# Performance work log

Measured on AMD Instinct MI355X. Metric: run time of the kernel, lower is better.

## Reference

```python
import math
import jax, jax.numpy as jnp
import numpy as np

EPS = 1e-8
N_ITER = 5


def _partial_ot(C, reg):
    # C: (M, N) cost matrix. Faithful to partial_optimal_transport with
    # diag-matmuls replaced by equivalent broadcast row/col scaling.
    M, N = C.shape
    a = jnp.full((M,), 1.0 / M, dtype=C.dtype)
    b = jnp.full((N,), 1.0 / N, dtype=C.dtype)
    m = jnp.minimum(a.sum(), b.sum())  # = 1.0 here
    K = jnp.exp(-C / jnp.clip(reg, EPS))
    K = K * (m / jnp.clip(K.sum(), EPS))

    def body(K, _):
        r = jnp.minimum(a / jnp.clip(K.sum(axis=1), EPS), 1.0)   # min(a/rowsum, dx)
        K1 = r[:, None] * K
        c = jnp.minimum(b / jnp.clip(K1.sum(axis=0), EPS), 1.0)  # min(b/colsum, dy)
        K2 = K1 * c[None, :]
        K = K2 * (m / jnp.clip(K2.sum(), EPS))
        return K, None

    K, _ = jax.lax.scan(body, K, None, length=N_ITER)
    return K


def _rigid_transform(a, b, w):
    # a: (M,3) source points, b: (M,3) weighted targets, w: (M,) weights
    wn = w[:, None] / (w.sum() + 1e-6)            # normalized weights (M,1)
    centroid_a = (a * wn).sum(axis=0)             # (3,)
    centroid_b = (b * wn).sum(axis=0)
    ac = a - centroid_a
    bc = b - centroid_b
    cov = ac.T @ (bc * wn)                        # (3,3)
    u, s, vh = jnp.linalg.svd(cov, full_matrices=False)
    v = vh.T                                      # torch.svd's V
    rot_pos = v @ u.T
    v_neg = v.at[:, 2].multiply(-1.0)
    rot_neg = v_neg @ u.T
    det = jnp.linalg.det(rot_pos)
    rot = jnp.where(det > 0, rot_pos, rot_neg)
    trans = -rot @ centroid_a + centroid_b        # (3,)
    return jnp.concatenate([rot, trans[:, None]], axis=1)  # (3,4)


def _one_sample(se, te, s, t, rho):
    # se: (D,M) src feats, te: (D,N) tgt feats, s: (3,M), t: (3,N)
    D = se.shape[0]
    scores = (se.T @ te) / math.sqrt(D)           # (M,N)
    C = -jax.nn.log_softmax(scores, axis=1)
    matches = _partial_ot(C, rho)                 # (M,N)
    rowsum = matches.sum(axis=1, keepdims=True)   # (M,1)
    weighted_ref = (matches @ t.T) / (rowsum + 1e-6)  # (M,3)
    T = _rigid_transform(s.T, weighted_ref, rowsum[:, 0])
    return T, matches


def _forward(src_embedding, tgt_embedding, src, tgt, rho):
    Ts, match_mats = jax.vmap(_one_sample, in_axes=(0, 0, 0, 0, None))(
        src_embedding, tgt_embedding, src, tgt, rho)
    return Ts[:, :3, :3], Ts[:, :3, 3], match_mats


def setup_inputs() -> dict:
    key = jax.random.key(0)
    k1, k2, k3, k4 = jax.random.split(key, 4)
    B, D, M, N = 16, 256, 2048, 2048
    return {
        "src_embedding": jax.random.normal(k1, (B, D, M), dtype=jnp.float32),
        "tgt_embedding": jax.random.normal(k2, (B, D, N), dtype=jnp.float32),
        "src": jax.random.normal(k3, (B, 3, M), dtype=jnp.float32),
        "tgt": jax.random.normal(k4, (B, 3, N), dtype=jnp.float32),
        "rho": jnp.asarray(1.0, dtype=jnp.float32),
    }


def reference(src_embedding, tgt_embedding, src, tgt, rho):
    return _forward(src_embedding, tgt_embedding, src, tgt, rho)
```

## Files before the change

kernel.cpp:

```cpp
#include <hip/hip_runtime.h>
#include <math.h>

#define B_ 16
#define D_ 256
#define M_ 2048
#define N_ 2048
#define EPSF 1e-8f
#define AVAL (1.0f/2048.0f)

typedef __bf16  bf16x8 __attribute__((ext_vector_type(8)));
typedef float   f32x4  __attribute__((ext_vector_type(4)));

__device__ __forceinline__ float wredsum(float x){
  #pragma unroll
  for (int off=32; off; off>>=1) x += __shfl_xor(x, off);
  return x;
}
__device__ __forceinline__ float wredmax(float x){
  #pragma unroll
  for (int off=32; off; off>>=1) x = fmaxf(x, __shfl_xor(x, off));
  return x;
}
__device__ __forceinline__ unsigned short f2bf(float x){
  unsigned int v = __float_as_uint(x);
  unsigned int r = (v + 0x7fffu + ((v>>16)&1u)) >> 16;
  return (unsigned short)r;
}
__device__ __forceinline__ float bf2f(unsigned short u){ return __uint_as_float(((unsigned int)u)<<16); }
__device__ __forceinline__ float h2f(unsigned short h){
  _Float16 x; __builtin_memcpy(&x,&h,2); return (float)x;
}
__device__ __forceinline__ unsigned short f2h(float x){
  _Float16 h = (_Float16)x; unsigned short u; __builtin_memcpy(&u,&h,2); return u;
}

__device__ __forceinline__ void gll16(const void* gsrc, void* ldst){
  __builtin_amdgcn_global_load_lds(
      (const __attribute__((address_space(1))) unsigned int*)gsrc,
      (__attribute__((address_space(3))) unsigned int*)(unsigned int)(unsigned long long)ldst,
      16, 0, 0);
}

__global__ __launch_bounds__(256) void convert_kernel(const float* __restrict__ se,
                                                      const float* __restrict__ te,
                                                      uint4* __restrict__ Ah, uint4* __restrict__ Al,
                                                      uint4* __restrict__ Bh, uint4* __restrict__ Bl)
{
  const int t  = threadIdx.x;
  const int mb = blockIdx.x;
  const int g  = blockIdx.y;
  const int z  = blockIdx.z;
  const int b  = z & 15, op = z >> 4;
  const int m  = mb*256 + t;
  const float* src = (op ? te : se) + (size_t)b*D_*M_ + (size_t)g*8*M_ + m;
  float x[8];
  #pragma unroll
  for (int j=0;j<8;j++) x[j] = src[(size_t)j*M_];
  unsigned int hw[4], lw[4];
  #pragma unroll
  for (int p=0;p<4;p++){
    float a0 = x[2*p], a1 = x[2*p+1];
    unsigned short h0 = f2bf(a0), h1 = f2bf(a1);
    unsigned short q0 = f2bf(a0 - bf2f(h0)), q1 = f2bf(a1 - bf2f(h1));
    hw[p] = (unsigned)h0 | ((unsigned)h1<<16);
    lw[p] = (unsigned)q0 | ((unsigned)q1<<16);
  }
  const size_t gi = (size_t)(b*32 + g)*2048 + m;
  uint4* Ph = op ? Bh : Ah;
  uint4* Pl = op ? Bl : Al;
  Ph[gi] = *(const uint4*)hw;
  Pl[gi] = *(const uint4*)lw;
}

__global__ __launch_bounds__(256) void gemm_fast(const uint4* __restrict__ Ah,
                                                 const uint4* __restrict__ Al,
                                                 const uint4* __restrict__ Bh,
                                                 const uint4* __restrict__ Bl,
                                                 float* __restrict__ S)
{
  __shared__ unsigned int sAh[2048], sAl[2048], sBh[2048], sBl[2048];
  const int b  = blockIdx.z;
  const int mb = blockIdx.y;
  const int nb = blockIdx.x;
  const int t    = threadIdx.x;
  const int wave = t >> 6, lane = t & 63;
  const int wy = wave >> 1, wx = wave & 1;
  const int quad = lane >> 4, l15 = lane & 15;

  f32x4 acc[4][4] = {};

  for (int kc=0; kc<8; kc++){
    __syncthreads();
    #pragma unroll
    for (int r=0;r<2;r++){
      const int i  = r*256 + t;
      const int gq = i >> 7, m = i & 127;
      const size_t rowg = (size_t)(b*32 + kc*4 + gq)*2048;
      gll16(Ah + rowg + mb*128 + m, (char*)sAh + (size_t)i*16);
      gll16(Al + rowg + mb*128 + m, (char*)sAl + (size_t)i*16);
      gll16(Bh + rowg + nb*128 + m, (char*)sBh + (size_t)i*16);
      gll16(Bl + rowg + nb*128 + m, (char*)sBl + (size_t)i*16);
    }
    __syncthreads();
    bf16x8 ah[4], al[4], bh[4], bl[4];
    #pragma unroll
    for (int rt=0;rt<4;rt++){
      int ra = (quad*128 + wy*64 + rt*16 + l15)*4;
      int rb = (quad*128 + wx*64 + rt*16 + l15)*4;
      ah[rt] = *(const bf16x8*)&sAh[ra];
      al[rt] = *(const bf16x8*)&sAl[ra];
      bh[rt] = *(const bf16x8*)&sBh[rb];
      bl[rt] = *(const bf16x8*)&sBl[rb];
    }
    #pragma unroll
    for (int rt=0;rt<4;rt++)
      #pragma unroll
      for (int ct=0;ct<4;ct++){
        acc[rt][ct] = __builtin_amdgcn_mfma_f32_16x16x32_bf16(ah[rt], bh[ct], acc[rt][ct], 0,0,0);
        acc[rt][ct] = __builtin_amdgcn_mfma_f32_16x16x32_bf16(ah[rt], bl[ct], acc[rt][ct], 0,0,0);
        acc[rt][ct] = __builtin_amdgcn_mfma_f32_16x16x32_bf16(al[rt], bh[ct], acc[rt][ct], 0,0,0);
      }
  }
  const float sc = 0.0625f;
  #pragma unroll
  for (int rt=0;rt<4;rt++){
    #pragma unroll
    for (int r=0;r<4;r++){
      int m = mb*128 + wy*64 + rt*16 + quad*4 + r;
      float* rowp = S + (size_t)(b*M_ + m)*N_;
      #pragma unroll
      for (int ct=0;ct<4;ct++){
        int n = nb*128 + wx*64 + ct*16 + l15;
        rowp[n] = acc[rt][ct][r] * sc;
      }
    }
  }
}

__global__ __launch_bounds__(256) void gemm_kernel(const float* __restrict__ se,
                                                   const float* __restrict__ te,
                                                   float* __restrict__ S)
{
  __shared__ unsigned int Ah[2048], Al[2048], Bh[2048], Bl[2048];
  const int b  = blockIdx.z;
  const int mb = blockIdx.y;
  const int nb = blockIdx.x;
  const int t    = threadIdx.x;
  const int wave = t >> 6, lane = t & 63;
  const int wy = wave >> 1, wx = wave & 1;
  const int quad = lane >> 4, l15 = lane & 15;
  const int ml  = t & 127;
  const int dh  = t >> 7;

  f32x4 acc[4][4] = {};

  const float* Abase = se + (size_t)b*D_*M_ + mb*128 + ml;
  const float* Bbase = te + (size_t)b*D_*M_ + nb*128 + ml;

  for (int kc=0; kc<8; kc++){
    __syncthreads();
    {
      float x[16];
      #pragma unroll
      for (int j=0;j<16;j++) x[j] = Abase[(size_t)(kc*32 + dh*16 + j)*M_];
      #pragma unroll
      for (int gi=0; gi<2; gi++){
        unsigned int hw[4], lw[4];
        #pragma unroll
        for (int p=0;p<4;p++){
          float a0 = x[gi*8+2*p], a1 = x[gi*8+2*p+1];
          unsigned short h0 = f2bf(a0), h1 = f2bf(a1);
          unsigned short q0 = f2bf(a0 - bf2f(h0)), q1 = f2bf(a1 - bf2f(h1));
          hw[p] = (unsigned)h0 | ((unsigned)h1<<16);
          lw[p] = (unsigned)q0 | ((unsigned)q1<<16);
        }
        int idx = ((dh*2+gi)*128 + ml)*4;
        *(uint4*)&Ah[idx] = *(uint4*)hw;
        *(uint4*)&Al[idx] = *(uint4*)lw;
      }
    }
    {
      float x[16];
      #pragma unroll
      for (int j=0;j<16;j++) x[j] = Bbase[(size_t)(kc*32 + dh*16 + j)*M_];
      #pragma unroll
      for (int gi=0; gi<2; gi++){
        unsigned int hw[4], lw[4];
        #pragma unroll
        for (int p=0;p<4;p++){
          float a0 = x[gi*8+2*p], a1 = x[gi*8+2*p+1];
          unsigned short h0 = f2bf(a0), h1 = f2bf(a1);
          unsigned short q0 = f2bf(a0 - bf2f(h0)), q1 = f2bf(a1 - bf2f(h1));
          hw[p] = (unsigned)h0 | ((unsigned)h1<<16);
          lw[p] = (unsigned)q0 | ((unsigned)q1<<16);
        }
        int idx = ((dh*2+gi)*128 + ml)*4;
        *(uint4*)&Bh[idx] = *(uint4*)hw;
        *(uint4*)&Bl[idx] = *(uint4*)lw;
      }
    }
    __syncthreads();
    bf16x8 ah[4], al[4], bh[4], bl[4];
    #pragma unroll
    for (int rt=0;rt<4;rt++){
      int ra = (quad*128 + wy*64 + rt*16 + l15)*4;
      int rb = (quad*128 + wx*64 + rt*16 + l15)*4;
      ah[rt] = *(const bf16x8*)&Ah[ra];
      al[rt] = *(const bf16x8*)&Al[ra];
      bh[rt] = *(const bf16x8*)&Bh[rb];
      bl[rt] = *(const bf16x8*)&Bl[rb];
    }
    #pragma unroll
    for (int rt=0;rt<4;rt++)
      #pragma unroll
      for (int ct=0;ct<4;ct++){
        acc[rt][ct] = __builtin_amdgcn_mfma_f32_16x16x32_bf16(ah[rt], bh[ct], acc[rt][ct], 0,0,0);
        acc[rt][ct] = __builtin_amdgcn_mfma_f32_16x16x32_bf16(ah[rt], bl[ct], acc[rt][ct], 0,0,0);
        acc[rt][ct] = __builtin_amdgcn_mfma_f32_16x16x32_bf16(al[rt], bh[ct], acc[rt][ct], 0,0,0);
      }
  }
  const float sc = 0.0625f;
  #pragma unroll
  for (int rt=0;rt<4;rt++){
    #pragma unroll
    for (int r=0;r<4;r++){
      int m = mb*128 + wy*64 + rt*16 + quad*4 + r;
      float* rowp = S + (size_t)(b*M_ + m)*N_;
      #pragma unroll
      for (int ct=0;ct<4;ct++){
        int n = nb*128 + wx*64 + ct*16 + l15;
        rowp[n] = acc[rt][ct][r] * sc;
      }
    }
  }
}

__global__ __launch_bounds__(256) void stats_kernel(float* __restrict__ S,
                                                    const float* __restrict__ rho,
                                                    float* __restrict__ lse,
                                                    float* __restrict__ y0)
{
  const int b = blockIdx.y;
  const int m = blockIdx.x*4 + (threadIdx.x>>6);
  const int lane = threadIdx.x & 63;
  const float invrho = 1.0f / fmaxf(rho[0], EPSF);
  float* row = S + (size_t)(b*M_ + m)*N_;
  const float4* row4 = (const float4*)row;
  float4 vals[8];
  float mx = -3.4e38f;
  #pragma unroll
  for (int k=0;k<8;k++){
    float4 v = row4[lane + 64*k];
    vals[k] = v;
    mx = fmaxf(mx, fmaxf(fmaxf(v.x,v.y), fmaxf(v.z,v.w)));
  }
  mx = wredmax(mx);
  float e1=0.0f;
  #pragma unroll
  for (int k=0;k<8;k++){
    float4 v = vals[k];
    e1 += __expf(v.x-mx)+__expf(v.y-mx)+__expf(v.z-mx)+__expf(v.w-mx);
  }
  e1 = wredsum(e1);
  const float l = mx + __logf(e1);
  uint2* rowh2 = (uint2*)row;
  float y2 = 0.0f;
  #pragma unroll
  for (int k=0;k<8;k++){
    float4 v = vals[k];
    unsigned short h0 = f2h(__expf((v.x-l)*invrho));
    unsigned short h1 = f2h(__expf((v.y-l)*invrho));
    unsigned short h2 = f2h(__expf((v.z-l)*invrho));
    unsigned short h3 = f2h(__expf((v.w-l)*invrho));
    y2 += h2f(h0)+h2f(h1)+h2f(h2)+h2f(h3);
    uint2 pk;
    pk.x = (unsigned)h0 | ((unsigned)h1<<16);
    pk.y = (unsigned)h2 | ((unsigned)h3<<16);
    rowh2[lane + 64*k] = pk;
  }
  y2 = wredsum(y2);
  if (lane==0){
    lse[b*M_+m] = l;
    y0 [b*M_+m] = y2;
  }
}

__global__ __launch_bounds__(256) void init_kernel(const float* __restrict__ y0,
                                                   float* __restrict__ u, float* __restrict__ v,
                                                   float* __restrict__ w, float* __restrict__ g)
{
  const int b = blockIdx.x; const int t = threadIdx.x;
  float s = 0.0f;
  for (int i=t;i<M_;i+=256) s += y0[b*M_+i];
  s = wredsum(s);
  __shared__ float red[4];
  __shared__ float gsh;
  if ((t&63)==0) red[t>>6]=s;
  __syncthreads();
  if (t==0){
    float tot = red[0]+red[1]+red[2]+red[3];
    float gg = 1.0f / fmaxf(tot, EPSF);
    g[b]=gg; gsh=gg;
  }
  __syncthreads();
  float gg = gsh;
  for (int i=t;i<M_;i+=256){
    float rs = gg * y0[b*M_+i];
    u[b*M_+i] = fminf(AVAL / fmaxf(rs, EPSF), 1.0f);
    v[b*M_+i] = 1.0f;
    w[b*M_+i] = 0.0f;
  }
}

__global__ __launch_bounds__(256) void col_kernel(const float* __restrict__ S,
                                                  const float* __restrict__ u,
                                                  float* __restrict__ w)
{
  const int b  = blockIdx.y;
  const int i0 = blockIdx.x*64;
  const int t  = threadIdx.x;
  float acc[8];
  #pragma unroll
  for (int k=0;k<8;k++) acc[k]=0.0f;
  for (int i=0;i<64;i++){
    int r = i0+i;
    float ui = u[b*M_+r];
    uint4 su = ((const uint4*)(S + (size_t)(b*M_ + r)*N_))[t];
    acc[0] += ui*h2f((unsigned short)(su.x&0xffff));
    acc[1] += ui*h2f((unsigned short)(su.x>>16));
    acc[2] += ui*h2f((unsigned short)(su.y&0xffff));
    acc[3] += ui*h2f((unsigned short)(su.y>>16));
    acc[4] += ui*h2f((unsigned short)(su.z&0xffff));
    acc[5] += ui*h2f((unsigned short)(su.z>>16));
    acc[6] += ui*h2f((unsigned short)(su.w&0xffff));
    acc[7] += ui*h2f((unsigned short)(su.w>>16));
  }
  #pragma unroll
  for (int k=0;k<8;k++) atomicAdd(&w[b*N_+t*8+k], acc[k]);
}

__global__ __launch_bounds__(256) void fused_rc_kernel(const float* __restrict__ S,
                                                       const float* __restrict__ vv,
                                                       float* __restrict__ u,
                                                       float* __restrict__ w,
                                                       const float* __restrict__ g)
{
  __shared__ float wsh[4][2048];
  const int b   = blockIdx.y;
  const int i0  = blockIdx.x*64;
  const int t   = threadIdx.x;
  const int wid = t>>6, lane = t&63;
  const float gg = g[b];
  const float4* vp = (const float4*)(vv + (size_t)b*N_);

  float acc[32];
  #pragma unroll
  for (int k=0;k<32;k++) acc[k]=0.0f;

  for (int r=0;r<16;r++){
    const int m = i0 + wid*16 + r;
    const uint4* rowh = (const uint4*)(S + (size_t)(b*M_ + m)*N_);
    float sv[32];
    float dot = 0.0f;
    #pragma unroll
    for (int k=0;k<4;k++){
      uint4 su  = rowh[lane + 64*k];
      float4 v0 = vp[(lane+64*k)*2];
      float4 v1 = vp[(lane+64*k)*2+1];
      float s0 = h2f((unsigned short)(su.x&0xffff));
      float s1 = h2f((unsigned short)(su.x>>16));
      float s2 = h2f((unsigned short)(su.y&0xffff));
      float s3 = h2f((unsigned short)(su.y>>16));
      float s4 = h2f((unsigned short)(su.z&0xffff));
      float s5 = h2f((unsigned short)(su.z>>16));
      float s6 = h2f((unsigned short)(su.w&0xffff));
      float s7 = h2f((unsigned short)(su.w>>16));
      dot += s0*v0.x + s1*v0.y + s2*v0.z + s3*v0.w
           + s4*v1.x + s5*v1.y + s6*v1.z + s7*v1.w;
      sv[k*8+0]=s0; sv[k*8+1]=s1; sv[k*8+2]=s2; sv[k*8+3]=s3;
      sv[k*8+4]=s4; sv[k*8+5]=s5; sv[k*8+6]=s6; sv[k*8+7]=s7;
    }
    dot = wredsum(dot);
    float ui = u[b*M_+m];
    float rs = gg*ui*dot;
    float un = ui * fminf(AVAL / fmaxf(rs, EPSF), 1.0f);
    if (lane==0) u[b*M_+m] = un;
    #pragma unroll
    for (int k=0;k<32;k++) acc[k] += un * sv[k];
  }

  #pragma unroll
  for (int k=0;k<4;k++){
    #pragma unroll
    for (int e=0;e<8;e++)
      wsh[wid][(lane+64*k)*8+e] = acc[k*8+e];
  }
  __syncthreads();
  #pragma unroll
  for (int e=0;e<8;e++){
    int j = t*8+e;
    float s = wsh[0][j]+wsh[1][j]+wsh[2][j]+wsh[3][j];
    atomicAdd(&w[b*N_+j], s);
  }
}

__global__ __launch_bounds__(256) void vupd_kernel(float* __restrict__ w,
                                                   float* __restrict__ v,
                                                   float* __restrict__ g)
{
  const int b = blockIdx.x; const int t = threadIdx.x;
  const float gg = g[b];
  float part = 0.0f;
  for (int i=t;i<N_;i+=256){
    float wj = w[b*N_+i];
    float vj = v[b*N_+i];
    float c  = fminf(AVAL/fmaxf(gg*vj*wj,EPSF), 1.0f);
    vj *= c;
    v[b*N_+i]=vj;
    part += wj*vj;
    w[b*N_+i]=0.0f;
  }
  part = wredsum(part);
  __shared__ float red[4];
  if ((t&63)==0) red[t>>6]=part;
  __syncthreads();
  if (t==0){
    float tot = gg*(red[0]+red[1]+red[2]+red[3]);
    g[b] = gg / fmaxf(tot, EPSF);
  }
}

__global__ __launch_bounds__(256) void final_kernel(float* __restrict__ S,
                                                    const float* __restrict__ u,
                                                    const float* __restrict__ v,
                                                    const float* __restrict__ g,
                                                    const float* __restrict__ tgt,
                                                    float* __restrict__ rowsum,
                                                    float* __restrict__ wref)
{
  const int b = blockIdx.y;
  const int m = blockIdx.x*4 + (threadIdx.x>>6);
  const int lane = threadIdx.x & 63;
  const float gu = g[b]*u[b*M_+m];
  float* row = S + (size_t)(b*M_ + m)*N_;
  const uint4* rowh = (const uint4*)row;
  uint4 su[4];
  #pragma unroll
  for (int k=0;k<4;k++) su[k] = rowh[lane + 64*k];
  __builtin_amdgcn_s_waitcnt(0);
  float4* rowf = (float4*)row;
  const float4* vp = (const float4*)(v + (size_t)b*N_);
  const float4* t0 = (const float4*)(tgt + ((size_t)b*3+0)*N_);
  const float4* t1 = (const float4*)(tgt + ((size_t)b*3+1)*N_);
  const float4* t2 = (const float4*)(tgt + ((size_t)b*3+2)*N_);
  float rs=0.0f, a0=0.0f, a1=0.0f, a2=0.0f;
  #pragma unroll
  for (int k=0;k<4;k++){
    float s[8] = {h2f((unsigned short)(su[k].x&0xffff)), h2f((unsigned short)(su[k].x>>16)),
                  h2f((unsigned short)(su[k].y&0xffff)), h2f((unsigned short)(su[k].y>>16)),
                  h2f((unsigned short)(su[k].z&0xffff)), h2f((unsigned short)(su[k].z>>16)),
                  h2f((unsigned short)(su[k].w&0xffff)), h2f((unsigned short)(su[k].w>>16))};
    int i2 = (lane+64*k)*2;
    #pragma unroll
    for (int h=0;h<2;h++){
      float4 v4 = vp[i2+h];
      float4 q0 = t0[i2+h], q1 = t1[i2+h], q2 = t2[i2+h];
      float m0 = gu*s[h*4+0]*v4.x;
      float m1 = gu*s[h*4+1]*v4.y;
      float m2 = gu*s[h*4+2]*v4.z;
      float m3 = gu*s[h*4+3]*v4.w;
      rs += m0+m1+m2+m3;
      a0 += m0*q0.x + m1*q0.y + m2*q0.z + m3*q0.w;
      a1 += m0*q1.x + m1*q1.y + m2*q1.z + m3*q1.w;
      a2 += m0*q2.x + m1*q2.y + m2*q2.z + m3*q2.w;
      rowf[i2+h] = make_float4(m0,m1,m2,m3);
    }
  }
  rs = wredsum(rs); a0=wredsum(a0); a1=wredsum(a1); a2=wredsum(a2);
  if (lane==0){
    rowsum[b*M_+m] = rs;
    float inv = 1.0f/(rs+1e-6f);
    size_t o = ((size_t)b*M_+m)*3;
    wref[o]=a0*inv; wref[o+1]=a1*inv; wref[o+2]=a2*inv;
  }
}

__device__ __forceinline__ void mat3_svd_rot(const float cov[3][3], float R[3][3])
{
  float mx = 1e-30f;
  for (int p=0;p<3;p++) for (int q=0;q<3;q++) mx = fmaxf(mx, fabsf(cov[p][q]));
  const float inv = 1.0f/mx;
  float Cm[3][3];
  for (int p=0;p<3;p++) for (int q=0;q<3;q++) Cm[p][q]=cov[p][q]*inv;
  float G[3][3];
  for (int p=0;p<3;p++)
    for (int q=0;q<3;q++)
      G[p][q] = Cm[0][p]*Cm[0][q] + Cm[1][p]*Cm[1][q] + Cm[2][p]*Cm[2][q];
  float V[3][3] = {{1,0,0},{0,1,0},{0,0,1}};
  const int PP[3]={0,0,1}, QQ[3]={1,2,2};
  for (int sweep=0;sweep<12;sweep++){
    for (int r=0;r<3;r++){
      int p=PP[r], q=QQ[r];
      float apq = G[p][q];
      if (fabsf(apq) < 1e-20f) continue;
      float tau = (G[q][q]-G[p][p])/(2.0f*apq);
      float tt  = (tau>=0.0f?1.0f:-1.0f)/(fabsf(tau)+sqrtf(1.0f+tau*tau));
      float cc  = 1.0f/sqrtf(1.0f+tt*tt);
      float ss  = tt*cc;
      for (int k=0;k<3;k++){ float gkp=G[k][p], gkq=G[k][q]; G[k][p]=cc*gkp-ss*gkq; G[k][q]=ss*gkp+cc*gkq; }
      for (int k=0;k<3;k++){ float gpk=G[p][k], gqk=G[q][k]; G[p][k]=cc*gpk-ss*gqk; G[q][k]=ss*gpk+cc*gqk; }
      for (int k=0;k<3;k++){ float vkp=V[k][p], vkq=V[k][q]; V[k][p]=cc*vkp-ss*vkq; V[k][q]=ss*vkp+cc*vkq; }
    }
  }
  float ev[3]={G[0][0],G[1][1],G[2][2]};
  int i0=0,i1=1,i2=2,tmp;
  if (ev[i0]<ev[i1]){tmp=i0;i0=i1;i1=tmp;}
  if (ev[i0]<ev[i2]){tmp=i0;i0=i2;i2=tmp;}
  if (ev[i1]<ev[i2]){tmp=i1;i1=i2;i2=tmp;}
  const int idx[3]={i0,i1,i2};
  float Vs[3][3];
  for (int k=0;k<3;k++) for (int i=0;i<3;i++) Vs[i][k]=V[i][idx[k]];
  float U[3][3]; float nrm[3];
  for (int k=0;k<3;k++){
    float ux = Cm[0][0]*Vs[0][k]+Cm[0][1]*Vs[1][k]+Cm[0][2]*Vs[2][k];
    float uy = Cm[1][0]*Vs[0][k]+Cm[1][1]*Vs[1][k]+Cm[1][2]*Vs[2][k];
    float uz = Cm[2][0]*Vs[0][k]+Cm[2][1]*Vs[1][k]+Cm[2][2]*Vs[2][k];
    float n = sqrtf(ux*ux+uy*uy+uz*uz);
    nrm[k]=n;
    float in = (n>1e-20f)?1.0f/n:0.0f;
    U[0][k]=ux*in; U[1][k]=uy*in; U[2][k]=uz*in;
  }
  if (nrm[2] < 1e-6f*fmaxf(nrm[0],1e-20f)){
    U[0][2]=U[1][0]*U[2][1]-U[2][0]*U[1][1];
    U[1][2]=U[2][0]*U[0][1]-U[0][0]*U[2][1];
    U[2][2]=U[0][0]*U[1][1]-U[1][0]*U[0][1];
  }
  float detC = Cm[0][0]*(Cm[1][1]*Cm[2][2]-Cm[1][2]*Cm[2][1])
             - Cm[0][1]*(Cm[1][0]*Cm[2][2]-Cm[1][2]*Cm[2][0])
             + Cm[0][2]*(Cm[1][0]*Cm[2][1]-Cm[1][1]*Cm[2][0]);
  float d2 = (detC>0.0f)?1.0f:-1.0f;
  for (int p=0;p<3;p++)
    for (int q=0;q<3;q++)
      R[p][q] = Vs[p][0]*U[q][0] + Vs[p][1]*U[q][1] + d2*Vs[p][2]*U[q][2];
}

__global__ __launch_bounds__(256) void rigid_kernel(const float* __restrict__ src,
                                                    const float* __restrict__ wref,
                                                    const float* __restrict__ rowsum,
                                                    float* __restrict__ out)
{
  const int b = blockIdx.x; const int t = threadIdx.x;
  float acc[16];
  #pragma unroll
  for (int k=0;k<16;k++) acc[k]=0.0f;
  for (int i=t;i<M_;i+=256){
    float wgt = rowsum[b*M_+i];
    float ax = src[((size_t)b*3+0)*M_+i];
    float ay = src[((size_t)b*3+1)*M_+i];
    float az = src[((size_t)b*3+2)*M_+i];
    const float* wr = wref + ((size_t)b*M_+i)*3;
    float bx=wr[0], by=wr[1], bz=wr[2];
    acc[0]+=wgt;
    acc[1]+=wgt*ax; acc[2]+=wgt*ay; acc[3]+=wgt*az;
    acc[4]+=wgt*bx; acc[5]+=wgt*by; acc[6]+=wgt*bz;
    acc[7] +=wgt*ax*bx; acc[8] +=wgt*ax*by; acc[9] +=wgt*ax*bz;
    acc[10]+=wgt*ay*bx; acc[11]+=wgt*ay*by; acc[12]+=wgt*ay*bz;
    acc[13]+=wgt*az*bx; acc[14]+=wgt*az*by; acc[15]+=wgt*az*bz;
  }
  __shared__ float red[4][16];
  const int wid = t>>6, lane = t&63;
  #pragma unroll
  for (int k=0;k<16;k++){
    float v = acc[k];
    #pragma unroll
    for (int off=32; off; off>>=1) v += __shfl_xor(v, off);
    if (lane==0) red[wid][k]=v;
  }
  __syncthreads();
  if (t==0){
    float s[16];
    #pragma unroll
    for (int k=0;k<16;k++) s[k]=red[0][k]+red[1][k]+red[2][k]+red[3][k];
    float wsum = s[0];
    float denom = wsum + 1e-6f;
    float ca[3]={s[1]/denom, s[2]/denom, s[3]/denom};
    float cb[3]={s[4]/denom, s[5]/denom, s[6]/denom};
    float sw = wsum/denom;
    float cov[3][3];
    for (int p=0;p<3;p++)
      for (int q=0;q<3;q++)
        cov[p][q] = s[7+p*3+q]/denom + (sw-2.0f)*ca[p]*cb[q];
    float R[3][3];
    mat3_svd_rot(cov, R);
    float tr[3];
    for (int p=0;p<3;p++)
      tr[p] = -(R[p][0]*ca[0]+R[p][1]*ca[1]+R[p][2]*ca[2]) + cb[p];
    for (int p=0;p<3;p++)
      for (int q=0;q<3;q++)
        out[b*9 + p*3 + q] = R[p][q];
    for (int p=0;p<3;p++)
      out[144 + b*3 + p] = tr[p];
  }
}

extern "C" void kernel_launch(void* const* d_in, const int* in_sizes, int n_in,
                              void* d_out, int out_size, void* d_ws, size_t ws_size,
                              hipStream_t stream)
{
  const float* se  = (const float*)d_in[0];
  const float* te  = (const float*)d_in[1];
  const float* src = (const float*)d_in[2];
  const float* tgt = (const float*)d_in[3];
  const float* rho = (const float*)d_in[4];
  float* out = (float*)d_out;
  float* S   = out + 192;
  float* ws  = (float*)d_ws;
  float* lse = ws;
  float* y0  = ws + 32768;
  float* u   = ws + 65536;
  float* v   = ws + 98304;
  float* w   = ws + 131072;
  float* g   = ws + 163840;
  float* wref= ws + 163904;

  const size_t PLANE_G     = (size_t)16*32*2048;
  const size_t PLANE_BYTES = PLANE_G*16;
  const size_t PLANE_OFF   = 1048832;
  const size_t need        = PLANE_OFF + 4*PLANE_BYTES;

  if (ws_size >= need){
    uint4* Ah = (uint4*)((char*)d_ws + PLANE_OFF);
    uint4* Al = Ah + PLANE_G;
    uint4* Bh = Al + PLANE_G;
    uint4* Bl = Bh + PLANE_G;
    convert_kernel<<<dim3(8,32,32),256,0,stream>>>(se,te,Ah,Al,Bh,Bl);
    gemm_fast     <<<dim3(16,16,16),256,0,stream>>>(Ah,Al,Bh,Bl,S);
  } else {
    gemm_kernel   <<<dim3(16,16,16),256,0,stream>>>(se,te,S);
  }
  stats_kernel<<<dim3(512,16),  256,0,stream>>>(S,rho,lse,y0);
  init_kernel <<<dim3(16),      256,0,stream>>>(y0,u,v,w,g);
  col_kernel <<<dim3(32,16),256,0,stream>>>(S,u,w);
  vupd_kernel<<<dim3(16),   256,0,stream>>>(w,v,g);
  for (int it=1; it<5; ++it){
    fused_rc_kernel<<<dim3(32,16),256,0,stream>>>(S,v,u,w,g);
    vupd_kernel    <<<dim3(16),   256,0,stream>>>(w,v,g);
  }
  final_kernel<<<dim3(512,16),256,0,stream>>>(S,u,v,g,tgt,y0,wref);
  rigid_kernel<<<dim3(16),    256,0,stream>>>(src,wref,y0,out);
}
```

Measured before the change: 835.4 us.

## Fuse Sinkhorn iterations into one persistent kernel with per-batch grid barriers

Replaces init, col, four fused row/col and five vupd launches with a single persistent sinkhorn kernel. Each of 32 chunks per batch keeps u in registers and v in LDS, and the chunks synchronise through per-batch atomic spin barriers. Separate w buffers per iteration are zeroed inside convert_kernel, which removes the zeroing work from vupd. This saves roughly ten kernel launches and their global round trips. The cost is a reliance on all 512 blocks being co-resident, plus spin-wait overhead and redundant v updates computed in every block.

```diff
diff --git a/kernel.cpp b/kernel.cpp
--- a/kernel.cpp
+++ b/kernel.cpp
@@ -7,6 +7,7 @@
 #define N_ 2048
 #define EPSF 1e-8f
 #define AVAL (1.0f/2048.0f)
+#define NCH 32
 
 typedef __bf16  bf16x8 __attribute__((ext_vector_type(8)));
 typedef float   f32x4  __attribute__((ext_vector_type(4)));
@@ -44,13 +45,19 @@
 __global__ __launch_bounds__(256) void convert_kernel(const float* __restrict__ se,
                                                       const float* __restrict__ te,
                                                       uint4* __restrict__ Ah, uint4* __restrict__ Al,
-                                                      uint4* __restrict__ Bh, uint4* __restrict__ Bl)
+                                                      uint4* __restrict__ Bh, uint4* __restrict__ Bl,
+                                                      float* __restrict__ zbase, int zcount)
 {
   const int t  = threadIdx.x;
   const int mb = blockIdx.x;
   const int g  = blockIdx.y;
   const int z  = blockIdx.z;
   const int b  = z & 15, op = z >> 4;
+  const int zb = blockIdx.x + 8*(blockIdx.y + 32*blockIdx.z);
+  {
+    int idx = zb*256 + t;
+    if (idx < zcount) zbase[idx] = 0.0f;
+  }
   const int m  = mb*256 + t;
   const float* src = (op ? te : se) + (size_t)b*D_*M_ + (size_t)g*8*M_ + m;
   float x[8];
@@ -70,6 +77,11 @@
   uint4* Pl = op ? Bl : Al;
   Ph[gi] = *(const uint4*)hw;
   Pl[gi] = *(const uint4*)lw;
+}
+
+__global__ __launch_bounds__(256) void zero_kernel(float* __restrict__ p, int n){
+  int i = blockIdx.x*256 + threadIdx.x;
+  if (i < n) p[i] = 0.0f;
 }
 
 __global__ __launch_bounds__(256) void gemm_fast(const uint4* __restrict__ Ah,
@@ -237,7 +249,6 @@
 
 __global__ __launch_bounds__(256) void stats_kernel(float* __restrict__ S,
                                                     const float* __restrict__ rho,
-                                                    float* __restrict__ lse,
                                                     float* __restrict__ y0)
 {
   const int b = blockIdx.y;
@@ -279,154 +290,177 @@
     rowh2[lane + 64*k] = pk;
   }
   y2 = wredsum(y2);
+  if (lane==0) y0[b*M_+m] = y2;
+}
+
+#define VIDX(j) ((j) + (((j)>>5)<<2))
+
+__device__ __forceinline__ void batch_barrier(unsigned int* ctr){
+  __syncthreads();
+  if (threadIdx.x==0){
+    __hip_atomic_fetch_add(ctr, 1u, __ATOMIC_RELEASE, __HIP_MEMORY_SCOPE_AGENT);
+    while (__hip_atomic_load(ctr, __ATOMIC_ACQUIRE, __HIP_MEMORY_SCOPE_AGENT) < NCH)
+      __builtin_amdgcn_s_sleep(2);
+  }
+  __syncthreads();
+}
+
+__global__ __launch_bounds__(256, 2) void sinkhorn_kernel(const float* __restrict__ S,
+                                                          const float* __restrict__ y0,
+                                                          float* __restrict__ u,
+                                                          float* __restrict__ v,
+                                                          float* __restrict__ g,
+                                                          float* __restrict__ wbuf,
+                                                          unsigned int* __restrict__ bar)
+{
+  __shared__ float vloc[2304];
+  __shared__ float wsh[4][2048];
+  __shared__ float redsh[4];
+  const int b = blockIdx.y, chunk = blockIdx.x;
+  const int t = threadIdx.x, wid = t>>6, lane = t&63;
+  const int i0 = chunk*64;
+
+  float s0 = 0.0f;
+  for (int i=t;i<N_;i+=256) s0 += y0[b*M_+i];
+  s0 = wredsum(s0);
+  if (lane==0) redsh[wid]=s0;
+  __syncthreads();
+  float gcur = 1.0f / fmaxf(redsh[0]+redsh[1]+redsh[2]+redsh[3], EPSF);
+  float u_w[16];
+  #pragma unroll
+  for (int r=0;r<16;r++){
+    float ys = y0[b*M_ + i0 + wid*16 + r];
+    u_w[r] = fminf(AVAL / fmaxf(gcur*ys, EPSF), 1.0f);
+  }
+  for (int i=t;i<N_;i+=256) vloc[VIDX(i)] = 1.0f;
+
+  float acc[32];
+
+  #pragma unroll
+  for (int k=0;k<32;k++) acc[k]=0.0f;
+  for (int r=0;r<16;r++){
+    const uint4* rowh = (const uint4*)(S + (size_t)(b*M_ + i0 + wid*16 + r)*N_);
+    const float un = u_w[r];
+    #pragma unroll
+    for (int k=0;k<4;k++){
+      uint4 su = rowh[lane + 64*k];
+      acc[k*8+0] += un*h2f((unsigned short)(su.x&0xffff));
+      acc[k*8+1] += un*h2f((unsigned short)(su.x>>16));
+      acc[k*8+2] += un*h2f((unsigned short)(su.y&0xffff));
+      acc[k*8+3] += un*h2f((unsigned short)(su.y>>16));
+      acc[k*8+4] += un*h2f((unsigned short)(su.z&0xffff));
+      acc[k*8+5] += un*h2f((unsigned short)(su.z>>16));
+      acc[k*8+6] += un*h2f((unsigned short)(su.w&0xffff));
+      acc[k*8+7] += un*h2f((unsigned short)(su.w>>16));
+    }
+  }
+  {
+    #pragma unroll
+    for (int k=0;k<4;k++)
+      #pragma unroll
+      for (int e=0;e<8;e++)
+        wsh[wid][(lane+64*k)*8+e] = acc[k*8+e];
+    __syncthreads();
+    float* w0 = wbuf + b*N_;
+    #pragma unroll
+    for (int e=0;e<8;e++){
+      int j = t*8+e;
+      atomicAdd(&w0[j], wsh[0][j]+wsh[1][j]+wsh[2][j]+wsh[3][j]);
+    }
+  }
+  batch_barrier(&bar[b*8 + 0]);
+
+  for (int it=1; it<=4; ++it){
+    const float* wprev = wbuf + (size_t)(it-1)*B_*N_ + b*N_;
+    float part = 0.0f;
+    for (int i=t;i<N_;i+=256){
+      float wj = __hip_atomic_load(&wprev[i], __ATOMIC_RELAXED, __HIP_MEMORY_SCOPE_AGENT);
+      float vj = vloc[VIDX(i)];
+      float c  = fminf(AVAL / fmaxf(gcur*vj*wj, EPSF), 1.0f);
+      vj *= c;
+      vloc[VIDX(i)] = vj;
+      part += wj*vj;
+    }
+    part = wredsum(part);
+    if (lane==0) redsh[wid]=part;
+    __syncthreads();
+    {
+      float tot = gcur*(redsh[0]+redsh[1]+redsh[2]+redsh[3]);
+      gcur = gcur / fmaxf(tot, EPSF);
+    }
+    #pragma unroll
+    for (int k=0;k<32;k++) acc[k]=0.0f;
+    for (int r=0;r<16;r++){
+      const uint4* rowh = (const uint4*)(S + (size_t)(b*M_ + i0 + wid*16 + r)*N_);
+      float sv[32];
+      float dot = 0.0f;
+      #pragma unroll
+      for (int k=0;k<4;k++){
+        uint4 su = rowh[lane + 64*k];
+        const int pb = VIDX((lane+64*k)*8);
+        float4 v0 = *(const float4*)&vloc[pb];
+        float4 v1 = *(const float4*)&vloc[pb+4];
+        float q0 = h2f((unsigned short)(su.x&0xffff));
+        float q1 = h2f((unsigned short)(su.x>>16));
+        float q2 = h2f((unsigned short)(su.y&0xffff));
+        float q3 = h2f((unsigned short)(su.y>>16));
+        float q4 = h2f((unsigned short)(su.z&0xffff));
+        float q5 = h2f((unsigned short)(su.z>>16));
+        float q6 = h2f((unsigned short)(su.w&0xffff));
+        float q7 = h2f((unsigned short)(su.w>>16));
+        dot += q0*v0.x + q1*v0.y + q2*v0.z + q3*v0.w
+             + q4*v1.x + q5*v1.y + q6*v1.z + q7*v1.w;
+        sv[k*8+0]=q0; sv[k*8+1]=q1; sv[k*8+2]=q2; sv[k*8+3]=q3;
+        sv[k*8+4]=q4; sv[k*8+5]=q5; sv[k*8+6]=q6; sv[k*8+7]=q7;
+      }
+      dot = wredsum(dot);
+      float ui = u_w[r];
+      float rs = gcur*ui*dot;
+      float un = ui * fminf(AVAL / fmaxf(rs, EPSF), 1.0f);
+      u_w[r] = un;
+      #pragma unroll
+      for (int k=0;k<32;k++) acc[k] += un * sv[k];
+    }
+    __syncthreads();
+    #pragma unroll
+    for (int k=0;k<4;k++)
+      #pragma unroll
+      for (int e=0;e<8;e++)
+        wsh[wid][(lane+64*k)*8+e] = acc[k*8+e];
+    __syncthreads();
+    float* wcur = wbuf + (size_t)it*B_*N_ + b*N_;
+    #pragma unroll
+    for (int e=0;e<8;e++){
+      int j = t*8+e;
+      atomicAdd(&wcur[j], wsh[0][j]+wsh[1][j]+wsh[2][j]+wsh[3][j]);
+    }
+    batch_barrier(&bar[b*8 + it]);
+  }
+
+  {
+    const float* wprev = wbuf + (size_t)4*B_*N_ + b*N_;
+    float part = 0.0f;
+    for (int i=t;i<N_;i+=256){
+      float wj = __hip_atomic_load(&wprev[i], __ATOMIC_RELAXED, __HIP_MEMORY_SCOPE_AGENT);
+      float vj = vloc[VIDX(i)];
+      float c  = fminf(AVAL / fmaxf(gcur*vj*wj, EPSF), 1.0f);
+      vj *= c;
+      vloc[VIDX(i)] = vj;
+      part += wj*vj;
+    }
+    part = wredsum(part);
+    if (lane==0) redsh[wid]=part;
+    __syncthreads();
+    float tot = gcur*(redsh[0]+redsh[1]+redsh[2]+redsh[3]);
+    gcur = gcur / fmaxf(tot, EPSF);
+  }
   if (lane==0){
-    lse[b*M_+m] = l;
-    y0 [b*M_+m] = y2;
-  }
-}
-
-__global__ __launch_bounds__(256) void init_kernel(const float* __restrict__ y0,
-                                                   float* __restrict__ u, float* __restrict__ v,
-                                                   float* __restrict__ w, float* __restrict__ g)
-{
-  const int b = blockIdx.x; const int t = threadIdx.x;
-  float s = 0.0f;
-  for (int i=t;i<M_;i+=256) s += y0[b*M_+i];
-  s = wredsum(s);
-  __shared__ float red[4];
-  __shared__ float gsh;
-  if ((t&63)==0) red[t>>6]=s;
-  __syncthreads();
-  if (t==0){
-    float tot = red[0]+red[1]+red[2]+red[3];
-    float gg = 1.0f / fmaxf(tot, EPSF);
-    g[b]=gg; gsh=gg;
-  }
-  __syncthreads();
-  float gg = gsh;
-  for (int i=t;i<M_;i+=256){
-    float rs = gg * y0[b*M_+i];
-    u[b*M_+i] = fminf(AVAL / fmaxf(rs, EPSF), 1.0f);
-    v[b*M_+i] = 1.0f;
-    w[b*M_+i] = 0.0f;
-  }
-}
-
-__global__ __launch_bounds__(256) void col_kernel(const float* __restrict__ S,
-                                                  const float* __restrict__ u,
-                                                  float* __restrict__ w)
-{
-  const int b  = blockIdx.y;
-  const int i0 = blockIdx.x*64;
-  const int t  = threadIdx.x;
-  float acc[8];
-  #pragma unroll
-  for (int k=0;k<8;k++) acc[k]=0.0f;
-  for (int i=0;i<64;i++){
-    int r = i0+i;
-    float ui = u[b*M_+r];
-    uint4 su = ((const uint4*)(S + (size_t)(b*M_ + r)*N_))[t];
-    acc[0] += ui*h2f((unsigned short)(su.x&0xffff));
-    acc[1] += ui*h2f((unsigned short)(su.x>>16));
-    acc[2] += ui*h2f((unsigned short)(su.y&0xffff));
-    acc[3] += ui*h2f((unsigned short)(su.y>>16));
-    acc[4] += ui*h2f((unsigned short)(su.z&0xffff));
-    acc[5] += ui*h2f((unsigned short)(su.z>>16));
-    acc[6] += ui*h2f((unsigned short)(su.w&0xffff));
-    acc[7] += ui*h2f((unsigned short)(su.w>>16));
-  }
-  #pragma unroll
-  for (int k=0;k<8;k++) atomicAdd(&w[b*N_+t*8+k], acc[k]);
-}
-
-__global__ __launch_bounds__(256) void fused_rc_kernel(const float* __restrict__ S,
-                                                       const float* __restrict__ vv,
-                                                       float* __restrict__ u,
-                                                       float* __restrict__ w,
-                                                       const float* __restrict__ g)
-{
-  __shared__ float wsh[4][2048];
-  const int b   = blockIdx.y;
-  const int i0  = blockIdx.x*64;
-  const int t   = threadIdx.x;
-  const int wid = t>>6, lane = t&63;
-  const float gg = g[b];
-  const float4* vp = (const float4*)(vv + (size_t)b*N_);
-
-  float acc[32];
-  #pragma unroll
-  for (int k=0;k<32;k++) acc[k]=0.0f;
-
-  for (int r=0;r<16;r++){
-    const int m = i0 + wid*16 + r;
-    const uint4* rowh = (const uint4*)(S + (size_t)(b*M_ + m)*N_);
-    float sv[32];
-    float dot = 0.0f;
-    #pragma unroll
-    for (int k=0;k<4;k++){
-      uint4 su  = rowh[lane + 64*k];
-      float4 v0 = vp[(lane+64*k)*2];
-      float4 v1 = vp[(lane+64*k)*2+1];
-      float s0 = h2f((unsigned short)(su.x&0xffff));
-      float s1 = h2f((unsigned short)(su.x>>16));
-      float s2 = h2f((unsigned short)(su.y&0xffff));
-      float s3 = h2f((unsigned short)(su.y>>16));
-      float s4 = h2f((unsigned short)(su.z&0xffff));
-      float s5 = h2f((unsigned short)(su.z>>16));
-      float s6 = h2f((unsigned short)(su.w&0xffff));
-      float s7 = h2f((unsigned short)(su.w>>16));
-      dot += s0*v0.x + s1*v0.y + s2*v0.z + s3*v0.w
-           + s4*v1.x + s5*v1.y + s6*v1.z + s7*v1.w;
-      sv[k*8+0]=s0; sv[k*8+1]=s1; sv[k*8+2]=s2; sv[k*8+3]=s3;
-      sv[k*8+4]=s4; sv[k*8+5]=s5; sv[k*8+6]=s6; sv[k*8+7]=s7;
-    }
-    dot = wredsum(dot);
-    float ui = u[b*M_+m];
-    float rs = gg*ui*dot;
-    float un = ui * fminf(AVAL / fmaxf(rs, EPSF), 1.0f);
-    if (lane==0) u[b*M_+m] = un;
-    #pragma unroll
-    for (int k=0;k<32;k++) acc[k] += un * sv[k];
-  }
-
-  #pragma unroll
-  for (int k=0;k<4;k++){
-    #pragma unroll
-    for (int e=0;e<8;e++)
-      wsh[wid][(lane+64*k)*8+e] = acc[k*8+e];
-  }
-  __syncthreads();
-  #pragma unroll
-  for (int e=0;e<8;e++){
-    int j = t*8+e;
-    float s = wsh[0][j]+wsh[1][j]+wsh[2][j]+wsh[3][j];
-    atomicAdd(&w[b*N_+j], s);
-  }
-}
-
-__global__ __launch_bounds__(256) void vupd_kernel(float* __restrict__ w,
-                                                   float* __restrict__ v,
-                                                   float* __restrict__ g)
-{
-  const int b = blockIdx.x; const int t = threadIdx.x;
-  const float gg = g[b];
-  float part = 0.0f;
-  for (int i=t;i<N_;i+=256){
-    float wj = w[b*N_+i];
-    float vj = v[b*N_+i];
-    float c  = fminf(AVAL/fmaxf(gg*vj*wj,EPSF), 1.0f);
-    vj *= c;
-    v[b*N_+i]=vj;
-    part += wj*vj;
-    w[b*N_+i]=0.0f;
-  }
-  part = wredsum(part);
-  __shared__ float red[4];
-  if ((t&63)==0) red[t>>6]=part;
-  __syncthreads();
-  if (t==0){
-    float tot = gg*(red[0]+red[1]+red[2]+red[3]);
-    g[b] = gg / fmaxf(tot, EPSF);
+    #pragma unroll
+    for (int r=0;r<16;r++) u[b*M_ + i0 + wid*16 + r] = u_w[r];
+  }
+  if (chunk==0){
+    for (int i=t;i<N_;i+=256) v[b*N_+i] = vloc[VIDX(i)];
+    if (t==0) g[b] = gcur;
   }
 }
 
@@ -615,17 +649,20 @@
   float* out = (float*)d_out;
   float* S   = out + 192;
   float* ws  = (float*)d_ws;
-  float* lse = ws;
-  float* y0  = ws + 32768;
-  float* u   = ws + 65536;
-  float* v   = ws + 98304;
-  float* w   = ws + 131072;
-  float* g   = ws + 163840;
-  float* wref= ws + 163904;
+
+  float*        y0   = ws;
+  float*        u    = ws + 32768;
+  float*        v    = ws + 65536;
+  float*        g    = ws + 98304;
+  float*        wref = ws + 98320;
+  float*        wbuf = ws + 196624;
+  unsigned int* bar  = (unsigned int*)(ws + 360464);
+  const int     ZCNT = 163840 + 128;
+  float*        zb   = wbuf;
 
   const size_t PLANE_G     = (size_t)16*32*2048;
   const size_t PLANE_BYTES = PLANE_G*16;
-  const size_t PLANE_OFF   = 1048832;
+  const size_t PLANE_OFF   = (size_t)360592*4;
   const size_t need        = PLANE_OFF + 4*PLANE_BYTES;
 
   if (ws_size >= need){
@@ -633,19 +670,14 @@
     uint4* Al = Ah + PLANE_G;
     uint4* Bh = Al + PLANE_G;
     uint4* Bl = Bh + PLANE_G;
-    convert_kernel<<<dim3(8,32,32),256,0,stream>>>(se,te,Ah,Al,Bh,Bl);
+    convert_kernel<<<dim3(8,32,32),256,0,stream>>>(se,te,Ah,Al,Bh,Bl,zb,ZCNT);
     gemm_fast     <<<dim3(16,16,16),256,0,stream>>>(Ah,Al,Bh,Bl,S);
   } else {
+    zero_kernel   <<<dim3((ZCNT+255)/256),256,0,stream>>>(zb,ZCNT);
     gemm_kernel   <<<dim3(16,16,16),256,0,stream>>>(se,te,S);
   }
-  stats_kernel<<<dim3(512,16),  256,0,stream>>>(S,rho,lse,y0);
-  init_kernel <<<dim3(16),      256,0,stream>>>(y0,u,v,w,g);
-  col_kernel <<<dim3(32,16),256,0,stream>>>(S,u,w);
-  vupd_kernel<<<dim3(16),   256,0,stream>>>(w,v,g);
-  for (int it=1; it<5; ++it){
-    fused_rc_kernel<<<dim3(32,16),256,0,stream>>>(S,v,u,w,g);
-    vupd_kernel    <<<dim3(16),   256,0,stream>>>(w,v,g);
-  }
-  final_kernel<<<dim3(512,16),256,0,stream>>>(S,u,v,g,tgt,y0,wref);
-  rigid_kernel<<<dim3(16),    256,0,stream>>>(src,wref,y0,out);
-}
+  stats_kernel   <<<dim3(512,16),  256,0,stream>>>(S,rho,y0);
+  sinkhorn_kernel<<<dim3(NCH,16),  256,0,stream>>>(S,y0,u,v,g,wbuf,bar);
+  final_kernel   <<<dim3(512,16),  256,0,stream>>>(S,u,v,g,tgt,y0,wref);
+  rigid_kernel   <<<dim3(16),      256,0,stream>>>(src,wref,y0,out);
+}
```

Result: slower. 1.631 ms (+95.2%).
